# Performance work log

Hardware: AMD Instinct MI355X
Metric: run time of the kernel (lower is better)

## Reference

```python
import jax, jax.numpy as jnp
import numpy as np

# Dimensions
B = 8        # batch
T = 2048     # subtokens per sample
G = 1024     # pooled tokens (nodes + edges) per sample
NN = 600     # node slots per sample (seg_ids > 0)
NE = 424     # edge slots per sample (seg_ids < 0); NN + NE == G
D = 1024     # d_model == pretrained_dim (BART-large), so need_proj is False
V = 53587    # AMRBART vocab size
L = 2        # graph_layer_configs.nlayers


def setup_inputs() -> dict:
    key = jax.random.key(0)
    ks = jax.random.split(key, 8)
    scale = 0.02
    tokens_ids = jax.random.randint(ks[0], (B, T), 0, V, dtype=jnp.int32)
    # ragged token_splits encoded as segment ids; uniform groups of size T//G == 2
    token_group_ids = jnp.broadcast_to(
        jnp.arange(T, dtype=jnp.int32) // (T // G), (B, T))
    # seg_ids: +1 for node slots, -1 for edge slots (nodes-first layout, no pad)
    seg_ids = jnp.broadcast_to(
        jnp.concatenate([jnp.ones(NN, jnp.int32), -jnp.ones(NE, jnp.int32)]),
        (B, G))
    # torch-geometric style global edge index over batch-concatenated nodes
    src = jax.random.randint(ks[1], (B, NE), 0, NN, dtype=jnp.int32)
    dst = jax.random.randint(ks[2], (B, NE), 0, NN, dtype=jnp.int32)
    offs = (jnp.arange(B, dtype=jnp.int32) * NN)[:, None]
    edge_index = jnp.stack([(src + offs).reshape(-1), (dst + offs).reshape(-1)], 0)
    embedding_table = jax.random.normal(ks[3], (V, D), dtype=jnp.float32) * scale
    W_msg = jax.random.normal(ks[4], (L, D, D), dtype=jnp.float32) * scale
    W_upd = jax.random.normal(ks[5], (L, D, D), dtype=jnp.float32) * scale
    W_edge = jax.random.normal(ks[6], (L, D, D), dtype=jnp.float32) * scale
    return {"tokens_ids": tokens_ids, "token_group_ids": token_group_ids,
            "seg_ids": seg_ids, "edge_index": edge_index,
            "embedding_table": embedding_table,
            "W_msg": W_msg, "W_upd": W_upd, "W_edge": W_edge}


def reference(tokens_ids, token_group_ids, seg_ids, edge_index,
              embedding_table, W_msg, W_upd, W_edge):
    # 1) embedding lookup: [B, T, D]
    token_feats = embedding_table[tokens_ids]
    # 2) ragged subtoken mean-pool (torch.split + mean) via segment_sum
    seg_sum = jax.vmap(lambda x, ids: jax.ops.segment_sum(x, ids, num_segments=G))
    sums = seg_sum(token_feats, token_group_ids)                       # [B, G, D]
    counts = seg_sum(jnp.ones((B, T, 1), token_feats.dtype), token_group_ids)
    pooled = sums / jnp.maximum(counts, 1.0)                           # [B, G, D]
    # 3) gather node/edge feats (seg_ids layout is nodes-first, statically known)
    nodes = pooled[:, :NN].reshape(B * NN, D)
    edges = pooled[:, NN:].reshape(B * NE, D)
    src, dst = edge_index[0], edge_index[1]
    # 4) graph layers: edge-conditioned message passing with residuals
    for l in range(L):
        msg = jax.nn.relu((nodes[src] + edges) @ W_msg[l])             # [B*NE, D]
        agg = jax.ops.segment_sum(msg, dst, num_segments=B * NN)       # [B*NN, D]
        new_edges = edges + (nodes[src] + nodes[dst]) @ W_edge[l]
        nodes = nodes + agg @ W_upd[l]
        edges = new_edges
    # 5) scatter back into padded [B, G, D] tensor (boolean-mask scatter in torch)
    all_feats = jnp.concatenate(
        [nodes.reshape(B, NN, D), edges.reshape(B, NE, D)], axis=1)
    return all_feats
```

## Files before the change

### kernel.cpp

```cpp
#include <hip/hip_runtime.h>

constexpr int kB  = 8;
constexpr int kT  = 2048;
constexpr int kG  = 1024;
constexpr int kNN = 600;
constexpr int kNE = 424;
constexpr int kD  = 1024;
constexpr int kL  = 2;
constexpr int kBNN = kB * kNN;
constexpr int kBNE = kB * kNE;
static_assert(kBNE % 64 == 0, "M tiles exact");

typedef __attribute__((ext_vector_type(4))) float f32x4;
typedef __attribute__((ext_vector_type(8))) short bf16x8;
typedef __attribute__((address_space(1))) const void gas_t;
typedef __attribute__((address_space(3))) void las_t;

__device__ __forceinline__ unsigned short f2bf(float x) {
    union { float f; unsigned u; } v; v.f = x;
    unsigned r = v.u + 0x7FFF + ((v.u >> 16) & 1);
    return (unsigned short)(r >> 16);
}

__device__ __forceinline__ void glds16(const void* g, void* l) {
    __builtin_amdgcn_global_load_lds((gas_t*)g, (las_t*)l, 16, 0, 0);
}

__device__ __forceinline__ size_t edge_out_off(int row) {
    int b = row / kNE, r = row - b * kNE;
    return ((size_t)(b * kG + kNN + r)) * kD;
}
__device__ __forceinline__ size_t node_out_off(int n) {
    int b = n / kNN, g = n - b * kNN;
    return ((size_t)(b * kG + g)) * kD;
}

__global__ __launch_bounds__(256) void prep_kernel(const int* __restrict__ tokens,
                                                   const int* __restrict__ gids,
                                                   const float* __restrict__ emb,
                                                   float* __restrict__ nodes,
                                                   float* __restrict__ edges,
                                                   const float* __restrict__ Wm,
                                                   const float* __restrict__ Wu,
                                                   const float* __restrict__ We,
                                                   unsigned short* __restrict__ Wt) {
    __shared__ float tbuf[32][33];
    int bx = blockIdx.x;
    if (bx < kB * kG) {
        int b = bx >> 10, g = bx & (kG - 1);
        int d = threadIdx.x * 4;
        const int* row = gids + (size_t)b * kT;
        int lo = 0, hi = kT;
        while (lo < hi) { int m = (lo + hi) >> 1; if (row[m] < g) lo = m + 1; else hi = m; }
        int s = lo; hi = kT;
        while (lo < hi) { int m = (lo + hi) >> 1; if (row[m] <= g) lo = m + 1; else hi = m; }
        int e = lo;
        float4 acc = make_float4(0.f, 0.f, 0.f, 0.f);
        for (int t = s; t < e; ++t) {
            int tok = tokens[(size_t)b * kT + t];
            const float4 v = *(const float4*)(emb + (size_t)tok * kD + d);
            acc.x += v.x; acc.y += v.y; acc.z += v.z; acc.w += v.w;
        }
        int c = e - s;
        float sc = 1.0f / (float)(c > 0 ? c : 1);
        acc.x *= sc; acc.y *= sc; acc.z *= sc; acc.w *= sc;
        float* dstp = (g < kNN)
            ? (nodes + (size_t)(b * kNN + g) * kD + d)
            : (edges + (size_t)(b * kNE + (g - kNN)) * kD + d);
        *(float4*)dstp = acc;
    } else {
        int idx = bx - kB * kG;
        int z = idx >> 10;
        int rem = idx & 1023;
        int n0 = (rem & 31) * 32, k0 = (rem >> 5) * 32;
        const float* W = (z < 2) ? (Wm + (size_t)z * kD * kD)
                       : (z < 4) ? (Wu + (size_t)(z - 2) * kD * kD)
                                 : (We + (size_t)(z - 4) * kD * kD);
        unsigned short* outp = Wt + (size_t)z * kD * kD;
        int r = threadIdx.x >> 3, c4 = (threadIdx.x & 7) * 4;
        const float4 v = *(const float4*)(W + (size_t)(k0 + r) * kD + n0 + c4);
        tbuf[r][c4] = v.x; tbuf[r][c4 + 1] = v.y; tbuf[r][c4 + 2] = v.z; tbuf[r][c4 + 3] = v.w;
        __syncthreads();
        ushort4 o;
        o.x = f2bf(tbuf[c4 + 0][r]); o.y = f2bf(tbuf[c4 + 1][r]);
        o.z = f2bf(tbuf[c4 + 2][r]); o.w = f2bf(tbuf[c4 + 3][r]);
        *(ushort4*)(outp + (size_t)(n0 + r) * kD + k0 + c4) = o;
    }
}

template <int COPY>
__global__ void gather_kernel(const float* __restrict__ nodes,
                              const float* __restrict__ edges,
                              const int* __restrict__ src,
                              const int* __restrict__ dst,
                              unsigned short* __restrict__ bufM,
                              unsigned short* __restrict__ bufE,
                              float* __restrict__ out) {
    int d = threadIdx.x * 4;
    int e = blockIdx.x;
    if (COPY && e >= kBNE) {
        int n = e - kBNE;
        *(float4*)(out + node_out_off(n) + d) =
            *(const float4*)(nodes + (size_t)n * kD + d);
        return;
    }
    int s = src[e], t = dst[e];
    const float4 a = *(const float4*)(nodes + (size_t)s * kD + d);
    const float4 b = *(const float4*)(edges + (size_t)e * kD + d);
    const float4 c = *(const float4*)(nodes + (size_t)t * kD + d);
    ushort4 om, oe;
    om.x = f2bf(a.x + b.x); om.y = f2bf(a.y + b.y);
    om.z = f2bf(a.z + b.z); om.w = f2bf(a.w + b.w);
    oe.x = f2bf(a.x + c.x); oe.y = f2bf(a.y + c.y);
    oe.z = f2bf(a.z + c.z); oe.w = f2bf(a.w + c.w);
    *(ushort4*)(bufM + (size_t)e * kD + d) = om;
    *(ushort4*)(bufE + (size_t)e * kD + d) = oe;
}

template <int MODE>
__device__ __forceinline__ void gemm_body(const unsigned short* __restrict__ A,
                                          const unsigned short* __restrict__ Wt,
                                          float* __restrict__ Cf,
                                          unsigned short* __restrict__ Cb,
                                          const float* __restrict__ Ef,
                                          const int* __restrict__ idxp,
                                          char* smem, int bn, int bm) {
    const int tid = threadIdx.x;
    const int lane = tid & 63;
    const int w = tid >> 6;
    const int wr = w >> 1, wc = w & 1;
    const int row0 = bm * 64, col0 = bn * 128;

    const unsigned short* agp = A + (size_t)(row0 + (tid >> 2)) * kD + (tid & 3) * 8;
    const unsigned short* bgp0 = Wt + (size_t)(col0 + (tid >> 2)) * kD + (tid & 3) * 8;
    const unsigned short* bgp1 = Wt + (size_t)(col0 + 64 + (tid >> 2)) * kD + (tid & 3) * 8;
    const int woff = w * 1024;
    auto stage = [&](int bsel, int k0) {
        char* base = smem + bsel * 12288 + woff;
        glds16(agp + k0, base);
        glds16(bgp0 + k0, base + 4096);
        glds16(bgp1 + k0, base + 8192);
    };

    constexpr int nt = kD / 32;
    stage(0, 0);
    stage(1, 32);

    f32x4 acc[2][4] = {};
    const int l15 = lane & 15, kg = lane >> 4;
    for (int t = 0; t < nt; ++t) {
        char* bufc = smem + (t & 1) * 12288;
        if (t < nt - 1) asm volatile("s_waitcnt vmcnt(3)" ::: "memory");
        else            asm volatile("s_waitcnt vmcnt(0)" ::: "memory");
        __builtin_amdgcn_s_barrier();
        bf16x8 af[2], bf[4];
#pragma unroll
        for (int i = 0; i < 2; ++i)
            af[i] = *(const bf16x8*)(bufc + ((wr * 32 + i * 16 + l15) * 32 + kg * 8) * 2);
#pragma unroll
        for (int j = 0; j < 4; ++j)
            bf[j] = *(const bf16x8*)(bufc + 4096 + ((wc * 64 + j * 16 + l15) * 32 + kg * 8) * 2);
        asm volatile("s_waitcnt lgkmcnt(0)" ::: "memory");
        __builtin_amdgcn_s_barrier();
        if (t + 2 < nt) stage(t & 1, (t + 2) * 32);
#pragma unroll
        for (int i = 0; i < 2; ++i)
#pragma unroll
            for (int j = 0; j < 4; ++j)
                acc[i][j] = __builtin_amdgcn_mfma_f32_16x16x32_bf16(af[i], bf[j], acc[i][j], 0, 0, 0);
    }
    const int lr = (lane >> 4) * 4;
#pragma unroll
    for (int i = 0; i < 2; ++i) {
        int rbase = row0 + wr * 32 + i * 16 + lr;
#pragma unroll
        for (int r = 0; r < 4; ++r) {
            int row = rbase + r;
            if (MODE == 0) {
                unsigned short* cp = Cb + (size_t)row * kD;
#pragma unroll
                for (int j = 0; j < 4; ++j) {
                    int col = col0 + wc * 64 + j * 16 + l15;
                    cp[col] = f2bf(fmaxf(acc[i][j][r], 0.f));
                }
            } else if (MODE == 1) {
                float* cp = Cf + (size_t)row * kD;
#pragma unroll
                for (int j = 0; j < 4; ++j) {
                    int col = col0 + wc * 64 + j * 16 + l15;
                    cp[col] += acc[i][j][r];
                }
            } else if (MODE == 2) {
                const float* ep = Ef + (size_t)row * kD;
                float* op = Cf + edge_out_off(row);
#pragma unroll
                for (int j = 0; j < 4; ++j) {
                    int col = col0 + wc * 64 + j * 16 + l15;
                    op[col] = ep[col] + acc[i][j][r];
                }
            } else if (MODE == 3) {
                float* cp = Cf + (size_t)idxp[row] * kD;
#pragma unroll
                for (int j = 0; j < 4; ++j) {
                    int col = col0 + wc * 64 + j * 16 + l15;
                    atomicAdd(cp + col, acc[i][j][r]);
                }
            } else {
                float* cp = Cf + node_out_off(idxp[row]);
#pragma unroll
                for (int j = 0; j < 4; ++j) {
                    int col = col0 + wc * 64 + j * 16 + l15;
                    atomicAdd(cp + col, acc[i][j][r]);
                }
            }
        }
    }
}

__global__ __launch_bounds__(256) void gemm_dual_l0(const unsigned short* __restrict__ A0,
                                                    const unsigned short* __restrict__ B0,
                                                    unsigned short* __restrict__ C0,
                                                    const unsigned short* __restrict__ A1,
                                                    const unsigned short* __restrict__ B1,
                                                    float* __restrict__ C1) {
    __shared__ char smem[24576];
    if (blockIdx.z == 0)
        gemm_body<0>(A0, B0, nullptr, C0, nullptr, nullptr, smem, blockIdx.x, blockIdx.y);
    else
        gemm_body<1>(A1, B1, C1, nullptr, nullptr, nullptr, smem, blockIdx.x, blockIdx.y);
}

__global__ __launch_bounds__(256) void gemm_dual_l1(const unsigned short* __restrict__ A0,
                                                    const unsigned short* __restrict__ B0,
                                                    unsigned short* __restrict__ C0,
                                                    const unsigned short* __restrict__ A1,
                                                    const unsigned short* __restrict__ B1,
                                                    float* __restrict__ outp,
                                                    const float* __restrict__ edges) {
    __shared__ char smem[24576];
    if (blockIdx.z == 0)
        gemm_body<0>(A0, B0, nullptr, C0, nullptr, nullptr, smem, blockIdx.x, blockIdx.y);
    else
        gemm_body<2>(A1, B1, outp, nullptr, edges, nullptr, smem, blockIdx.x, blockIdx.y);
}

__global__ __launch_bounds__(256) void gemm_upd_l0(const unsigned short* __restrict__ A,
                                                   const unsigned short* __restrict__ B,
                                                   float* __restrict__ C,
                                                   const int* __restrict__ dstIdx) {
    __shared__ char smem[24576];
    gemm_body<3>(A, B, C, nullptr, nullptr, dstIdx, smem, blockIdx.x, blockIdx.y);
}

__global__ __launch_bounds__(256) void gemm_upd_l1(const unsigned short* __restrict__ A,
                                                   const unsigned short* __restrict__ B,
                                                   float* __restrict__ outp,
                                                   const int* __restrict__ dstIdx) {
    __shared__ char smem[24576];
    gemm_body<4>(A, B, outp, nullptr, nullptr, dstIdx, smem, blockIdx.x, blockIdx.y);
}

extern "C" void kernel_launch(void* const* d_in, const int* in_sizes, int n_in,
                              void* d_out, int out_size, void* d_ws, size_t ws_size,
                              hipStream_t stream) {
    const int*   tokens = (const int*)d_in[0];
    const int*   gids   = (const int*)d_in[1];
    const int*   eidx   = (const int*)d_in[3];
    const float* emb    = (const float*)d_in[4];
    const float* Wm     = (const float*)d_in[5];
    const float* Wu     = (const float*)d_in[6];
    const float* We     = (const float*)d_in[7];
    float* out = (float*)d_out;

    constexpr size_t szNodes = (size_t)kBNN * kD * 4;
    constexpr size_t szEdges = (size_t)kBNE * kD * 4;
    constexpr size_t szBufM  = (size_t)kBNE * kD * 2;
    constexpr size_t szBufE  = (size_t)kBNE * kD * 2;
    constexpr size_t szMsgB  = (size_t)kBNE * kD * 2;
    char* ws = (char*)d_ws;
    float*          nodes = (float*)ws;
    float*          edges = (float*)(ws + szNodes);
    unsigned short* bufM  = (unsigned short*)(ws + szNodes + szEdges);
    unsigned short* bufE  = (unsigned short*)(ws + szNodes + szEdges + szBufM);
    unsigned short* msgb  = (unsigned short*)(ws + szNodes + szEdges + szBufM + szBufE);
    unsigned short* Wt    = (unsigned short*)(ws + szNodes + szEdges + szBufM + szBufE + szMsgB);

    const int* srcIdx = eidx;
    const int* dstIdx = eidx + kBNE;
    unsigned short* WtM = Wt;
    unsigned short* WtU = Wt + (size_t)2 * kD * kD;
    unsigned short* WtE = Wt + (size_t)4 * kD * kD;

    prep_kernel<<<kB * kG + 6 * 1024, 256, 0, stream>>>(
        tokens, gids, emb, nodes, edges, Wm, Wu, We, Wt);

    constexpr int mt = kBNE / 64;
    const dim3 gdual(kD / 128, mt, 2);
    const dim3 gupd(kD / 128, mt, 1);

    gather_kernel<0><<<kBNE, 256, 0, stream>>>(nodes, edges, srcIdx, dstIdx, bufM, bufE, out);
    gemm_dual_l0<<<gdual, 256, 0, stream>>>(bufM, WtM, msgb, bufE, WtE, edges);
    gemm_upd_l0<<<gupd, 256, 0, stream>>>(msgb, WtU, nodes, dstIdx);

    gather_kernel<1><<<kBNE + kBNN, 256, 0, stream>>>(nodes, edges, srcIdx, dstIdx, bufM, bufE, out);
    gemm_dual_l1<<<gdual, 256, 0, stream>>>(bufM, WtM + (size_t)kD * kD, msgb,
                                            bufE, WtE + (size_t)kD * kD, out, edges);
    gemm_upd_l1<<<gupd, 256, 0, stream>>>(msgb, WtU + (size_t)kD * kD, out, dstIdx);
}
```

Before: 166.5 us.

## Enlarge GEMM tile to 128x128 with fragment-major LDS layout and M-tail guard

Each GEMM block now computes a 128x128 output tile instead of 64x128, so each wave holds a 4x4 grid of MFMA accumulators and every loaded A/B fragment is reused across more MFMAs. Shared memory is laid out as 16-row fragment chunks whose loads match the MFMA register layout directly, and each thread issues four global-to-LDS loads per stage. Because 3392 rows is not a multiple of 128, A rows past the end are clamped on load and their stores are skipped. The trade-offs are fewer blocks per launch (27 row tiles instead of 53), more accumulator registers per thread and larger LDS, which may lower occupancy and leave some of the 256 CUs without work.

```diff
diff --git a/kernel.cpp b/kernel.cpp
--- a/kernel.cpp
+++ b/kernel.cpp
@@ -9,7 +9,6 @@
 constexpr int kL  = 2;
 constexpr int kBNN = kB * kNN;
 constexpr int kBNE = kB * kNE;
-static_assert(kBNE % 64 == 0, "M tiles exact");
 
 typedef __attribute__((ext_vector_type(4))) float f32x4;
 typedef __attribute__((ext_vector_type(8))) short bf16x8;
@@ -124,58 +123,68 @@
                                           unsigned short* __restrict__ Cb,
                                           const float* __restrict__ Ef,
                                           const int* __restrict__ idxp,
-                                          char* smem, int bn, int bm) {
+                                          int M, char* smem, int bn, int bm) {
     const int tid = threadIdx.x;
     const int lane = tid & 63;
     const int w = tid >> 6;
     const int wr = w >> 1, wc = w & 1;
-    const int row0 = bm * 64, col0 = bn * 128;
-
-    const unsigned short* agp = A + (size_t)(row0 + (tid >> 2)) * kD + (tid & 3) * 8;
-    const unsigned short* bgp0 = Wt + (size_t)(col0 + (tid >> 2)) * kD + (tid & 3) * 8;
-    const unsigned short* bgp1 = Wt + (size_t)(col0 + 64 + (tid >> 2)) * kD + (tid & 3) * 8;
-    const int woff = w * 1024;
+    const int row0 = bm * 128, col0 = bn * 128;
+    const int l15 = lane & 15, kg = lane >> 4;
+
+    const unsigned short* agp[2];
+    const unsigned short* bgp[2];
+    int lbase[2];
+#pragma unroll
+    for (int q = 0; q < 2; ++q) {
+        int chunk = q * 4 + w;
+        int arow = row0 + chunk * 16 + l15;
+        if (arow >= M) arow = M - 1;
+        agp[q] = A + (size_t)arow * kD + kg * 8;
+        bgp[q] = Wt + (size_t)(col0 + chunk * 16 + l15) * kD + kg * 8;
+        lbase[q] = chunk * 1024;
+    }
     auto stage = [&](int bsel, int k0) {
-        char* base = smem + bsel * 12288 + woff;
-        glds16(agp + k0, base);
-        glds16(bgp0 + k0, base + 4096);
-        glds16(bgp1 + k0, base + 8192);
+        char* base = smem + bsel * 16384;
+#pragma unroll
+        for (int q = 0; q < 2; ++q) {
+            glds16(agp[q] + k0, base + lbase[q]);
+            glds16(bgp[q] + k0, base + 8192 + lbase[q]);
+        }
     };
 
     constexpr int nt = kD / 32;
     stage(0, 0);
     stage(1, 32);
 
-    f32x4 acc[2][4] = {};
-    const int l15 = lane & 15, kg = lane >> 4;
+    f32x4 acc[4][4] = {};
     for (int t = 0; t < nt; ++t) {
-        char* bufc = smem + (t & 1) * 12288;
-        if (t < nt - 1) asm volatile("s_waitcnt vmcnt(3)" ::: "memory");
+        char* bufc = smem + (t & 1) * 16384;
+        if (t < nt - 1) asm volatile("s_waitcnt vmcnt(4)" ::: "memory");
         else            asm volatile("s_waitcnt vmcnt(0)" ::: "memory");
         __builtin_amdgcn_s_barrier();
-        bf16x8 af[2], bf[4];
-#pragma unroll
-        for (int i = 0; i < 2; ++i)
-            af[i] = *(const bf16x8*)(bufc + ((wr * 32 + i * 16 + l15) * 32 + kg * 8) * 2);
-#pragma unroll
-        for (int j = 0; j < 4; ++j)
-            bf[j] = *(const bf16x8*)(bufc + 4096 + ((wc * 64 + j * 16 + l15) * 32 + kg * 8) * 2);
+        bf16x8 af[4], bf[4];
+#pragma unroll
+        for (int i = 0; i < 4; ++i) {
+            af[i] = *(const bf16x8*)(bufc + (wr * 4 + i) * 1024 + kg * 256 + l15 * 16);
+            bf[i] = *(const bf16x8*)(bufc + 8192 + (wc * 4 + i) * 1024 + kg * 256 + l15 * 16);
+        }
         asm volatile("s_waitcnt lgkmcnt(0)" ::: "memory");
         __builtin_amdgcn_s_barrier();
         if (t + 2 < nt) stage(t & 1, (t + 2) * 32);
 #pragma unroll
-        for (int i = 0; i < 2; ++i)
+        for (int i = 0; i < 4; ++i)
 #pragma unroll
             for (int j = 0; j < 4; ++j)
                 acc[i][j] = __builtin_amdgcn_mfma_f32_16x16x32_bf16(af[i], bf[j], acc[i][j], 0, 0, 0);
     }
     const int lr = (lane >> 4) * 4;
 #pragma unroll
-    for (int i = 0; i < 2; ++i) {
-        int rbase = row0 + wr * 32 + i * 16 + lr;
+    for (int i = 0; i < 4; ++i) {
+        int rbase = row0 + wr * 64 + i * 16 + lr;
 #pragma unroll
         for (int r = 0; r < 4; ++r) {
             int row = rbase + r;
+            if (row >= M) continue;
             if (MODE == 0) {
                 unsigned short* cp = Cb + (size_t)row * kD;
 #pragma unroll
@@ -223,11 +232,11 @@
                                                     const unsigned short* __restrict__ A1,
                                                     const unsigned short* __restrict__ B1,
                                                     float* __restrict__ C1) {
-    __shared__ char smem[24576];
+    __shared__ char smem[32768];
     if (blockIdx.z == 0)
-        gemm_body<0>(A0, B0, nullptr, C0, nullptr, nullptr, smem, blockIdx.x, blockIdx.y);
+        gemm_body<0>(A0, B0, nullptr, C0, nullptr, nullptr, kBNE, smem, blockIdx.x, blockIdx.y);
     else
-        gemm_body<1>(A1, B1, C1, nullptr, nullptr, nullptr, smem, blockIdx.x, blockIdx.y);
+        gemm_body<1>(A1, B1, C1, nullptr, nullptr, nullptr, kBNE, smem, blockIdx.x, blockIdx.y);
 }
 
 __global__ __launch_bounds__(256) void gemm_dual_l1(const unsigned short* __restrict__ A0,
@@ -237,27 +246,27 @@
                                                     const unsigned short* __restrict__ B1,
                                                     float* __restrict__ outp,
                                                     const float* __restrict__ edges) {
-    __shared__ char smem[24576];
+    __shared__ char smem[32768];
     if (blockIdx.z == 0)
-        gemm_body<0>(A0, B0, nullptr, C0, nullptr, nullptr, smem, blockIdx.x, blockIdx.y);
+        gemm_body<0>(A0, B0, nullptr, C0, nullptr, nullptr, kBNE, smem, blockIdx.x, blockIdx.y);
     else
-        gemm_body<2>(A1, B1, outp, nullptr, edges, nullptr, smem, blockIdx.x, blockIdx.y);
+        gemm_body<2>(A1, B1, outp, nullptr, edges, nullptr, kBNE, smem, blockIdx.x, blockIdx.y);
 }
 
 __global__ __launch_bounds__(256) void gemm_upd_l0(const unsigned short* __restrict__ A,
                                                    const unsigned short* __restrict__ B,
                                                    float* __restrict__ C,
                                                    const int* __restrict__ dstIdx) {
-    __shared__ char smem[24576];
-    gemm_body<3>(A, B, C, nullptr, nullptr, dstIdx, smem, blockIdx.x, blockIdx.y);
+    __shared__ char smem[32768];
+    gemm_body<3>(A, B, C, nullptr, nullptr, dstIdx, kBNE, smem, blockIdx.x, blockIdx.y);
 }
 
 __global__ __launch_bounds__(256) void gemm_upd_l1(const unsigned short* __restrict__ A,
                                                    const unsigned short* __restrict__ B,
                                                    float* __restrict__ outp,
                                                    const int* __restrict__ dstIdx) {
-    __shared__ char smem[24576];
-    gemm_body<4>(A, B, outp, nullptr, nullptr, dstIdx, smem, blockIdx.x, blockIdx.y);
+    __shared__ char smem[32768];
+    gemm_body<4>(A, B, outp, nullptr, nullptr, dstIdx, kBNE, smem, blockIdx.x, blockIdx.y);
 }
 
 extern "C" void kernel_launch(void* const* d_in, const int* in_sizes, int n_in,
@@ -294,7 +303,7 @@
     prep_kernel<<<kB * kG + 6 * 1024, 256, 0, stream>>>(
         tokens, gids, emb, nodes, edges, Wm, Wu, We, Wt);
 
-    constexpr int mt = kBNE / 64;
+    constexpr int mt = (kBNE + 127) / 128;
     const dim3 gdual(kD / 128, mt, 2);
     const dim3 gupd(kD / 128, mt, 1);
 
```

Measured after the change: 193.4 us. 1.16x slower.
